# Kernel optimization log

Measured on AMD Instinct MI355X. Metric: run time of the kernel, lower is better.

Reference implementation:

```python
import jax, jax.numpy as jnp
import numpy as np

NUM_CLASSES = 32
N = 2_000_000
EPS = jnp.float32(np.finfo(np.float32).eps)  # torch.finfo(torch.float32).eps


def setup_inputs() -> dict:
    key = jax.random.key(0)
    k1, k2 = jax.random.split(key)
    y_true = jax.random.normal(k1, (N, NUM_CLASSES), dtype=jnp.float32)
    y_pred = jax.random.normal(k2, (N, NUM_CLASSES), dtype=jnp.float32)
    confusion_matrix = jnp.zeros((NUM_CLASSES, NUM_CLASSES), dtype=jnp.float32)
    return {"y_true": y_true, "y_pred": y_pred, "confusion_matrix": confusion_matrix}


def reference(y_true, y_pred, confusion_matrix):
    C = confusion_matrix.shape[0]
    # update(): argmax then scatter-accumulate into the confusion matrix
    t = jnp.argmax(y_true, axis=1)  # [N] int
    p = jnp.argmax(y_pred, axis=1)  # [N] int
    flat = t * C + p                # flattened (row, col) index
    hist = jnp.zeros((C * C,), dtype=jnp.float32).at[flat].add(1.0)
    cm = confusion_matrix + hist.reshape(C, C)
    # compute() with average='macro'
    tp = jnp.diag(cm)
    predicted_positives = jnp.sum(cm, axis=0)
    precision_per_class = tp / (predicted_positives + EPS)
    return jnp.mean(precision_per_class)
```

## Files before the change

kernel.cpp:

```cpp
#include <hip/hip_runtime.h>

#define C 32
#define BINS (C * C)
#define NBLOCKS 2048
#define NTHREADS 256
#define ROWS_PER_STEP ((NBLOCKS * NTHREADS) / 8)
#define FLT_EPS 1.1920928955078125e-07f

typedef float v4f __attribute__((ext_vector_type(4)));

__device__ __forceinline__ unsigned long long pack_best4(v4f v, int base) {
    unsigned long long best = 0ull;
    #pragma unroll
    for (int k = 0; k < 4; ++k) {
        unsigned int u = __float_as_uint(v[k]);
        unsigned int key = u ^ ((unsigned int)((int)u >> 31) | 0x80000000u);
        unsigned long long p =
            ((unsigned long long)key << 32) | (unsigned int)(63 - (base + k));
        best = (p > best) ? p : best;
    }
    return best;
}

__global__ __launch_bounds__(NTHREADS) void hist_kernel(
    const float* __restrict__ yt,
    const float* __restrict__ yp,
    unsigned int* __restrict__ partial,
    int N)
{
    __shared__ unsigned int lhist[BINS];
    const int t = threadIdx.x;
    for (int i = t; i < BINS; i += NTHREADS) lhist[i] = 0u;
    __syncthreads();

    const int lane8 = t & 7;
    long long row = (long long)((blockIdx.x * NTHREADS + t) >> 3);
    bool valid = row < N;
    v4f a, b;
    if (valid) {
        a = __builtin_nontemporal_load(((const v4f*)(yt + row * C)) + lane8);
        b = __builtin_nontemporal_load(((const v4f*)(yp + row * C)) + lane8);
    }

    while (valid) {
        const long long nrow = row + ROWS_PER_STEP;
        const bool nvalid = nrow < N;
        v4f na, nb;
        if (nvalid) {
            na = __builtin_nontemporal_load(((const v4f*)(yt + nrow * C)) + lane8);
            nb = __builtin_nontemporal_load(((const v4f*)(yp + nrow * C)) + lane8);
        }

        unsigned long long bt = pack_best4(a, lane8 * 4);
        unsigned long long bp = pack_best4(b, lane8 * 4);
        #pragma unroll
        for (int m = 1; m < 8; m <<= 1) {
            unsigned long long ot = __shfl_xor(bt, m);
            bt = (ot > bt) ? ot : bt;
            unsigned long long op = __shfl_xor(bp, m);
            bp = (op > bp) ? op : bp;
        }
        if (lane8 == 0) {
            const int ti = 63 - (int)(bt & 63ull);
            const int pi = 63 - (int)(bp & 63ull);
            atomicAdd(&lhist[ti * C + pi], 1u);
        }

        row = nrow; valid = nvalid; a = na; b = nb;
    }

    __syncthreads();
    if (t < 32) {
        unsigned int cs = 0;
        #pragma unroll
        for (int i = 0; i < C; ++i) cs += lhist[i * C + t];
        partial[(size_t)blockIdx.x * 64 + t] = cs;
    } else if (t < 64) {
        const int j = t - 32;
        partial[(size_t)blockIdx.x * 64 + t] = lhist[j * C + j];
    }
}

__global__ __launch_bounds__(1024) void finalize_kernel(
    const unsigned int* __restrict__ partial,
    const float* __restrict__ cm_in,
    float* __restrict__ out)
{
    __shared__ float sums[16][64];
    const int tid = threadIdx.x;
    const int col = tid & 63;
    const int kg = tid >> 6;

    unsigned int s = 0;
    #pragma unroll 8
    for (int k = kg * (NBLOCKS / 16); k < (kg + 1) * (NBLOCKS / 16); ++k)
        s += partial[(size_t)k * 64 + col];
    sums[kg][col] = (float)s;
    __syncthreads();

    if (tid < 64) {
        float tot = 0.0f;
        #pragma unroll
        for (int g = 0; g < 16; ++g) tot += sums[g][tid];
        sums[0][tid] = tot;
    }
    __syncthreads();

    if (tid < C) {
        const int j = tid;
        float pp = sums[0][j];
        float tp = sums[0][C + j];
        float cmcol = 0.0f;
        #pragma unroll
        for (int i = 0; i < C; ++i) cmcol += cm_in[i * C + j];
        pp += cmcol;
        tp += cm_in[j * C + j];
        float prec = tp / (pp + FLT_EPS);
        #pragma unroll
        for (int m = 1; m < C; m <<= 1) prec += __shfl_xor(prec, m);
        if (j == 0) out[0] = prec * (1.0f / (float)C);
    }
}

extern "C" void kernel_launch(void* const* d_in, const int* in_sizes, int n_in,
                              void* d_out, int out_size, void* d_ws, size_t ws_size,
                              hipStream_t stream)
{
    const float* yt = (const float*)d_in[0];
    const float* yp = (const float*)d_in[1];
    const float* cm = (const float*)d_in[2];
    float* out = (float*)d_out;
    const int N = in_sizes[0] / C;

    unsigned int* partial = (unsigned int*)d_ws;

    hist_kernel<<<NBLOCKS, NTHREADS, 0, stream>>>(yt, yp, partial, N);
    finalize_kernel<<<1, 1024, 0, stream>>>(partial, cm, out);
}
```

Measured before the change: 461.3 us.

## Replace 64-bit packed argmax with float max shuffles plus ballot; keep only column and diagonal counts

The argmax switches from shuffling packed 64-bit key/index pairs to shuffling 32-bit float maxima, then uses a ballot and find-first-set to recover the lowest index that holds the maximum. The full 1024-bin shared histogram becomes two 32-entry arrays for column sums and diagonal counts, which are the only values the finalize step reads. This halves shuffle traffic and removes the shared-memory clear and column reduction. Tie handling still picks the first index, but NaN behaviour may differ from the previous ordered-key comparison.

Result: no change. 466.1 us (+1.0%).

```diff
diff --git a/kernel.cpp b/kernel.cpp
--- a/kernel.cpp
+++ b/kernel.cpp
@@ -1,7 +1,6 @@
 #include <hip/hip_runtime.h>
 
 #define C 32
-#define BINS (C * C)
 #define NBLOCKS 2048
 #define NTHREADS 256
 #define ROWS_PER_STEP ((NBLOCKS * NTHREADS) / 8)
@@ -9,31 +8,23 @@
 
 typedef float v4f __attribute__((ext_vector_type(4)));
 
-__device__ __forceinline__ unsigned long long pack_best4(v4f v, int base) {
-    unsigned long long best = 0ull;
-    #pragma unroll
-    for (int k = 0; k < 4; ++k) {
-        unsigned int u = __float_as_uint(v[k]);
-        unsigned int key = u ^ ((unsigned int)((int)u >> 31) | 0x80000000u);
-        unsigned long long p =
-            ((unsigned long long)key << 32) | (unsigned int)(63 - (base + k));
-        best = (p > best) ? p : best;
-    }
-    return best;
-}
-
 __global__ __launch_bounds__(NTHREADS) void hist_kernel(
     const float* __restrict__ yt,
     const float* __restrict__ yp,
     unsigned int* __restrict__ partial,
     int N)
 {
-    __shared__ unsigned int lhist[BINS];
+    __shared__ unsigned int colcnt[C];
+    __shared__ unsigned int diagcnt[C];
     const int t = threadIdx.x;
-    for (int i = t; i < BINS; i += NTHREADS) lhist[i] = 0u;
+    if (t < C) colcnt[t] = 0u;
+    else if (t < 2 * C) diagcnt[t - C] = 0u;
     __syncthreads();
 
+    const int lane = t & 63;
     const int lane8 = t & 7;
+    const int gb = lane & ~7;
+
     long long row = (long long)((blockIdx.x * NTHREADS + t) >> 3);
     bool valid = row < N;
     v4f a, b;
@@ -51,33 +42,38 @@
             nb = __builtin_nontemporal_load(((const v4f*)(yp + nrow * C)) + lane8);
         }
 
-        unsigned long long bt = pack_best4(a, lane8 * 4);
-        unsigned long long bp = pack_best4(b, lane8 * 4);
+        const float lt = fmaxf(fmaxf(a.x, a.y), fmaxf(a.z, a.w));
+        const int it4 = (lt == a.x) ? 0 : (lt == a.y) ? 1 : (lt == a.z) ? 2 : 3;
+        const float lp = fmaxf(fmaxf(b.x, b.y), fmaxf(b.z, b.w));
+        const int ip4 = (lp == b.x) ? 0 : (lp == b.y) ? 1 : (lp == b.z) ? 2 : 3;
+
+        float mt = lt, mp = lp;
         #pragma unroll
         for (int m = 1; m < 8; m <<= 1) {
-            unsigned long long ot = __shfl_xor(bt, m);
-            bt = (ot > bt) ? ot : bt;
-            unsigned long long op = __shfl_xor(bp, m);
-            bp = (op > bp) ? op : bp;
+            mt = fmaxf(mt, __shfl_xor(mt, m));
+            mp = fmaxf(mp, __shfl_xor(mp, m));
         }
+
+        const unsigned long long bt = __ballot(lt == mt);
+        const unsigned long long bp = __ballot(lp == mp);
+        const int wlT = __ffsll((unsigned long long)((bt >> gb) & 0xFFull)) - 1;
+        const int wlP = __ffsll((unsigned long long)((bp >> gb) & 0xFFull)) - 1;
+        const int ti = wlT * 4 + __shfl(it4, gb + wlT);
+        const int pi = wlP * 4 + __shfl(ip4, gb + wlP);
+
         if (lane8 == 0) {
-            const int ti = 63 - (int)(bt & 63ull);
-            const int pi = 63 - (int)(bp & 63ull);
-            atomicAdd(&lhist[ti * C + pi], 1u);
+            atomicAdd(&colcnt[pi], 1u);
+            if (ti == pi) atomicAdd(&diagcnt[pi], 1u);
         }
 
         row = nrow; valid = nvalid; a = na; b = nb;
     }
 
     __syncthreads();
-    if (t < 32) {
-        unsigned int cs = 0;
-        #pragma unroll
-        for (int i = 0; i < C; ++i) cs += lhist[i * C + t];
-        partial[(size_t)blockIdx.x * 64 + t] = cs;
-    } else if (t < 64) {
-        const int j = t - 32;
-        partial[(size_t)blockIdx.x * 64 + t] = lhist[j * C + j];
+    if (t < C) {
+        partial[(size_t)blockIdx.x * 64 + t] = colcnt[t];
+    } else if (t < 2 * C) {
+        partial[(size_t)blockIdx.x * 64 + t] = diagcnt[t - C];
     }
 }
 
```
